# Kernel tuning notes

Measured on AMD Instinct MI355X. Metric: run time of the kernel, lower is better.

Reference implementation:

```python
import jax, jax.numpy as jnp
import numpy as np

N_IN = 100000
N_OUT = 5000
N_EDGES = 200000
FILTERS = 4
BATCH = 128


def setup_inputs() -> dict:
    key = jax.random.key(0)
    k1, k2, k3, k4 = jax.random.split(key, 4)
    x = jax.random.normal(k1, (BATCH, N_IN), dtype=jnp.float32)
    weight = jax.random.normal(k2, (N_EDGES, FILTERS), dtype=jnp.float32) * 0.01
    bias = jnp.zeros((N_OUT, FILTERS), dtype=jnp.float32)
    rows = jax.random.randint(k3, (N_EDGES,), 0, N_IN)
    cols = jax.random.randint(k4, (N_EDGES,), 0, N_OUT)
    return {"x": x, "weight": weight, "bias": bias, "rows": rows, "cols": cols}


def reference(x, weight, bias, rows, cols):
    # Sparse locally-connected layer: out[b,o,f] = sum_{e: cols[e]==o} x[b, rows[e]] * weight[e, f]
    # (equivalent to the original dense einsum 'bi,iof->bof' with the scattered weight tensor,
    #  but computed directly on the COO edge list)
    xg = x[:, rows]                                   # (B, E) gather per edge
    contrib = xg[:, :, None] * weight[None, :, :]     # (B, E, F)
    out = jnp.zeros((x.shape[0], N_OUT, FILTERS), dtype=x.dtype)
    out = out.at[:, cols, :].add(contrib)             # scatter-add to output nodes
    out = out + bias[None, :, :]
    return jax.nn.relu(out)
```

## Files before the change

kernel.cpp:

```cpp
#include <hip/hip_runtime.h>

#define N_IN 100000
#define N_OUT 5000
#define N_EDGES 200000
#define NB 128
#define CAP 128
#define T_TILES 3125
#define S_BLOCKS 782

__device__ __forceinline__ unsigned short f2bf_rne(float f) {
    unsigned int u = __float_as_uint(f);
    u += 0x7FFF + ((u >> 16) & 1);
    return (unsigned short)(u >> 16);
}

__global__ __launch_bounds__(256) void fused_prep(
    const float* __restrict__ x, unsigned short* __restrict__ xTb,
    const int* __restrict__ rows, const int* __restrict__ cols,
    int* __restrict__ count, int2* __restrict__ edge_pack) {
    __shared__ float tile[32][129];
    int t = threadIdx.x;
    if (blockIdx.x < T_TILES) {
        int n0 = blockIdx.x * 32;
        int q = t & 7;
        int brow = t >> 3;
#pragma unroll
        for (int p = 0; p < 4; ++p) {
            int b = brow + 32 * p;
            float4 v = *(const float4*)(x + (size_t)b * N_IN + n0 + 4 * q);
            tile[4 * q + 0][b] = v.x;
            tile[4 * q + 1][b] = v.y;
            tile[4 * q + 2][b] = v.z;
            tile[4 * q + 3][b] = v.w;
        }
        __syncthreads();
        int s = t & 31;
        int r = t >> 5;
#pragma unroll
        for (int p = 0; p < 4; ++p) {
            int nl = r + 8 * p;
            ushort4 o;
            o.x = f2bf_rne(tile[nl][4 * s + 0]);
            o.y = f2bf_rne(tile[nl][4 * s + 1]);
            o.z = f2bf_rne(tile[nl][4 * s + 2]);
            o.w = f2bf_rne(tile[nl][4 * s + 3]);
            *(ushort4*)(xTb + (size_t)(n0 + nl) * NB + 4 * s) = o;
        }
    } else {
        int e = (blockIdx.x - T_TILES) * 256 + t;
        if (e < N_EDGES) {
            int c = cols[e];
            int pos = atomicAdd(&count[c], 1);
            if (pos < CAP) edge_pack[c * CAP + pos] = make_int2(rows[e], e);
        }
    }
}

__device__ __forceinline__ void ld_step(unsigned int u, float4 wt, float4& a0, float4& a1) {
    float xa = __uint_as_float(u << 16);
    float xb = __uint_as_float(u & 0xFFFF0000u);
    a0.x = fmaf(xa, wt.x, a0.x); a0.y = fmaf(xa, wt.y, a0.y);
    a0.z = fmaf(xa, wt.z, a0.z); a0.w = fmaf(xa, wt.w, a0.w);
    a1.x = fmaf(xb, wt.x, a1.x); a1.y = fmaf(xb, wt.y, a1.y);
    a1.z = fmaf(xb, wt.z, a1.z); a1.w = fmaf(xb, wt.w, a1.w);
}

__global__ __launch_bounds__(256) void ld1d_main(
    const unsigned int* __restrict__ xg,
    const float4* __restrict__ bias4, const float4* __restrict__ w4,
    const int* __restrict__ count, const int2* __restrict__ edge_pack,
    float4* __restrict__ out4) {
    __shared__ int2 s_pack[4][CAP];
    int t = threadIdx.x;
    int wv = t >> 6;
    int l = t & 63;
    int c = blockIdx.x * 4 + wv;
    int cnt = count[c];
    cnt = (cnt < CAP) ? cnt : CAP;
    if (l < cnt) s_pack[wv][l] = edge_pack[c * CAP + l];
    if (l + 64 < cnt) s_pack[wv][l + 64] = edge_pack[c * CAP + l + 64];
    __syncthreads();
    float4 a0 = bias4[c];
    float4 a1 = a0;
    int k = 0;
    for (; k + 4 <= cnt; k += 4) {
        int2 p0 = s_pack[wv][k], p1 = s_pack[wv][k + 1];
        int2 p2 = s_pack[wv][k + 2], p3 = s_pack[wv][k + 3];
        unsigned int u0 = xg[(size_t)p0.x * 64 + l];
        unsigned int u1 = xg[(size_t)p1.x * 64 + l];
        unsigned int u2 = xg[(size_t)p2.x * 64 + l];
        unsigned int u3 = xg[(size_t)p3.x * 64 + l];
        float4 w0 = w4[p0.y], w1 = w4[p1.y], w2 = w4[p2.y], w3 = w4[p3.y];
        ld_step(u0, w0, a0, a1);
        ld_step(u1, w1, a0, a1);
        ld_step(u2, w2, a0, a1);
        ld_step(u3, w3, a0, a1);
    }
    for (; k < cnt; ++k) {
        int2 p = s_pack[wv][k];
        unsigned int u = xg[(size_t)p.x * 64 + l];
        float4 w = w4[p.y];
        ld_step(u, w, a0, a1);
    }
    a0.x = fmaxf(a0.x, 0.f); a0.y = fmaxf(a0.y, 0.f);
    a0.z = fmaxf(a0.z, 0.f); a0.w = fmaxf(a0.w, 0.f);
    a1.x = fmaxf(a1.x, 0.f); a1.y = fmaxf(a1.y, 0.f);
    a1.z = fmaxf(a1.z, 0.f); a1.w = fmaxf(a1.w, 0.f);
    out4[(size_t)(2 * l) * N_OUT + c] = a0;
    out4[(size_t)(2 * l + 1) * N_OUT + c] = a1;
}

extern "C" void kernel_launch(void* const* d_in, const int* in_sizes, int n_in,
                              void* d_out, int out_size, void* d_ws, size_t ws_size,
                              hipStream_t stream) {
    const float* x      = (const float*)d_in[0];
    const float* weight = (const float*)d_in[1];
    const float* bias   = (const float*)d_in[2];
    const int*   rows   = (const int*)d_in[3];
    const int*   cols   = (const int*)d_in[4];

    char* ws = (char*)d_ws;
    unsigned short* xTb  = (unsigned short*)(ws + 0);
    int2* edge_pack = (int2*)(ws + 25600000);
    int*  count     = (int*)(ws + 30720000);

    hipMemsetAsync(count, 0, N_OUT * sizeof(int), stream);

    fused_prep<<<T_TILES + S_BLOCKS, 256, 0, stream>>>(x, xTb, rows, cols, count, edge_pack);

    ld1d_main<<<N_OUT / 4, 256, 0, stream>>>((const unsigned int*)xTb, (const float4*)bias,
                                             (const float4*)weight, count, edge_pack,
                                             (float4*)d_out);
}
```

Before: 126.9 us.

## Split each output node across two wavefronts and reorder prep blocks

The main kernel now gives each output node two wavefronts that take alternate edges and combine partial sums through shared memory, with an 8-way unrolled gather loop. This doubles the block count and the memory-level parallelism per node, at the cost of an extra barrier and an LDS reduction. The prep kernel puts the edge-bucketing blocks first so the atomics start early, and it reads the transpose tile with float4 LDS loads using a padded stride of 132.

After: 131.4 us. 3.5% more time.

```diff
diff --git a/kernel.cpp b/kernel.cpp
--- a/kernel.cpp
+++ b/kernel.cpp
@@ -7,6 +7,7 @@
 #define CAP 128
 #define T_TILES 3125
 #define S_BLOCKS 782
+#define LDSW 132
 
 __device__ __forceinline__ unsigned short f2bf_rne(float f) {
     unsigned int u = __float_as_uint(f);
@@ -14,14 +15,30 @@
     return (unsigned short)(u >> 16);
 }
 
+__device__ __forceinline__ void ld_step(unsigned int u, float4 wt, float4& a0, float4& a1) {
+    float xa = __uint_as_float(u << 16);
+    float xb = __uint_as_float(u & 0xFFFF0000u);
+    a0.x = fmaf(xa, wt.x, a0.x); a0.y = fmaf(xa, wt.y, a0.y);
+    a0.z = fmaf(xa, wt.z, a0.z); a0.w = fmaf(xa, wt.w, a0.w);
+    a1.x = fmaf(xb, wt.x, a1.x); a1.y = fmaf(xb, wt.y, a1.y);
+    a1.z = fmaf(xb, wt.z, a1.z); a1.w = fmaf(xb, wt.w, a1.w);
+}
+
 __global__ __launch_bounds__(256) void fused_prep(
     const float* __restrict__ x, unsigned short* __restrict__ xTb,
     const int* __restrict__ rows, const int* __restrict__ cols,
     int* __restrict__ count, int2* __restrict__ edge_pack) {
-    __shared__ float tile[32][129];
+    __shared__ float tile[32][LDSW];
     int t = threadIdx.x;
-    if (blockIdx.x < T_TILES) {
-        int n0 = blockIdx.x * 32;
+    if (blockIdx.x < S_BLOCKS) {
+        int e = blockIdx.x * 256 + t;
+        if (e < N_EDGES) {
+            int c = cols[e];
+            int pos = atomicAdd(&count[c], 1);
+            if (pos < CAP) edge_pack[c * CAP + pos] = make_int2(rows[e], e);
+        }
+    } else {
+        int n0 = (blockIdx.x - S_BLOCKS) * 32;
         int q = t & 7;
         int brow = t >> 3;
 #pragma unroll
@@ -39,30 +56,15 @@
 #pragma unroll
         for (int p = 0; p < 4; ++p) {
             int nl = r + 8 * p;
+            float4 f = *(const float4*)&tile[nl][4 * s];
             ushort4 o;
-            o.x = f2bf_rne(tile[nl][4 * s + 0]);
-            o.y = f2bf_rne(tile[nl][4 * s + 1]);
-            o.z = f2bf_rne(tile[nl][4 * s + 2]);
-            o.w = f2bf_rne(tile[nl][4 * s + 3]);
+            o.x = f2bf_rne(f.x);
+            o.y = f2bf_rne(f.y);
+            o.z = f2bf_rne(f.z);
+            o.w = f2bf_rne(f.w);
             *(ushort4*)(xTb + (size_t)(n0 + nl) * NB + 4 * s) = o;
         }
-    } else {
-        int e = (blockIdx.x - T_TILES) * 256 + t;
-        if (e < N_EDGES) {
-            int c = cols[e];
-            int pos = atomicAdd(&count[c], 1);
-            if (pos < CAP) edge_pack[c * CAP + pos] = make_int2(rows[e], e);
-        }
     }
-}
-
-__device__ __forceinline__ void ld_step(unsigned int u, float4 wt, float4& a0, float4& a1) {
-    float xa = __uint_as_float(u << 16);
-    float xb = __uint_as_float(u & 0xFFFF0000u);
-    a0.x = fmaf(xa, wt.x, a0.x); a0.y = fmaf(xa, wt.y, a0.y);
-    a0.z = fmaf(xa, wt.z, a0.z); a0.w = fmaf(xa, wt.w, a0.w);
-    a1.x = fmaf(xb, wt.x, a1.x); a1.y = fmaf(xb, wt.y, a1.y);
-    a1.z = fmaf(xb, wt.z, a1.z); a1.w = fmaf(xb, wt.w, a1.w);
 }
 
 __global__ __launch_bounds__(256) void ld1d_main(
@@ -70,44 +72,68 @@
     const float4* __restrict__ bias4, const float4* __restrict__ w4,
     const int* __restrict__ count, const int2* __restrict__ edge_pack,
     float4* __restrict__ out4) {
-    __shared__ int2 s_pack[4][CAP];
+    __shared__ int2 s_pack[2][CAP];
+    __shared__ float4 s_part[2][64][2];
     int t = threadIdx.x;
-    int wv = t >> 6;
+    int w = t >> 6;
+    int cw = w >> 1;
+    int h = w & 1;
     int l = t & 63;
-    int c = blockIdx.x * 4 + wv;
+    int c = blockIdx.x * 2 + cw;
     int cnt = count[c];
     cnt = (cnt < CAP) ? cnt : CAP;
-    if (l < cnt) s_pack[wv][l] = edge_pack[c * CAP + l];
-    if (l + 64 < cnt) s_pack[wv][l + 64] = edge_pack[c * CAP + l + 64];
+    {
+        int idx = h * 64 + l;
+        if (idx < cnt) s_pack[cw][idx] = edge_pack[c * CAP + idx];
+    }
     __syncthreads();
-    float4 a0 = bias4[c];
-    float4 a1 = a0;
-    int k = 0;
-    for (; k + 4 <= cnt; k += 4) {
-        int2 p0 = s_pack[wv][k], p1 = s_pack[wv][k + 1];
-        int2 p2 = s_pack[wv][k + 2], p3 = s_pack[wv][k + 3];
+    float4 a0, a1;
+    if (h == 0) { a0 = bias4[c]; } else { a0 = make_float4(0.f, 0.f, 0.f, 0.f); }
+    a1 = a0;
+    int k = h;
+    for (; k + 14 < cnt; k += 16) {
+        int2 p0 = s_pack[cw][k],      p1 = s_pack[cw][k + 2];
+        int2 p2 = s_pack[cw][k + 4],  p3 = s_pack[cw][k + 6];
+        int2 p4 = s_pack[cw][k + 8],  p5 = s_pack[cw][k + 10];
+        int2 p6 = s_pack[cw][k + 12], p7 = s_pack[cw][k + 14];
         unsigned int u0 = xg[(size_t)p0.x * 64 + l];
         unsigned int u1 = xg[(size_t)p1.x * 64 + l];
         unsigned int u2 = xg[(size_t)p2.x * 64 + l];
         unsigned int u3 = xg[(size_t)p3.x * 64 + l];
+        unsigned int u4 = xg[(size_t)p4.x * 64 + l];
+        unsigned int u5 = xg[(size_t)p5.x * 64 + l];
+        unsigned int u6 = xg[(size_t)p6.x * 64 + l];
+        unsigned int u7 = xg[(size_t)p7.x * 64 + l];
         float4 w0 = w4[p0.y], w1 = w4[p1.y], w2 = w4[p2.y], w3 = w4[p3.y];
-        ld_step(u0, w0, a0, a1);
-        ld_step(u1, w1, a0, a1);
-        ld_step(u2, w2, a0, a1);
-        ld_step(u3, w3, a0, a1);
+        float4 wq = w4[p4.y], w5 = w4[p5.y], w6 = w4[p6.y], w7 = w4[p7.y];
+        ld_step(u0, w0, a0, a1); ld_step(u1, w1, a0, a1);
+        ld_step(u2, w2, a0, a1); ld_step(u3, w3, a0, a1);
+        ld_step(u4, wq, a0, a1); ld_step(u5, w5, a0, a1);
+        ld_step(u6, w6, a0, a1); ld_step(u7, w7, a0, a1);
     }
-    for (; k < cnt; ++k) {
-        int2 p = s_pack[wv][k];
+    for (; k < cnt; k += 2) {
+        int2 p = s_pack[cw][k];
         unsigned int u = xg[(size_t)p.x * 64 + l];
-        float4 w = w4[p.y];
-        ld_step(u, w, a0, a1);
+        float4 wt = w4[p.y];
+        ld_step(u, wt, a0, a1);
     }
-    a0.x = fmaxf(a0.x, 0.f); a0.y = fmaxf(a0.y, 0.f);
-    a0.z = fmaxf(a0.z, 0.f); a0.w = fmaxf(a0.w, 0.f);
-    a1.x = fmaxf(a1.x, 0.f); a1.y = fmaxf(a1.y, 0.f);
-    a1.z = fmaxf(a1.z, 0.f); a1.w = fmaxf(a1.w, 0.f);
-    out4[(size_t)(2 * l) * N_OUT + c] = a0;
-    out4[(size_t)(2 * l + 1) * N_OUT + c] = a1;
+    if (h == 1) {
+        s_part[cw][l][0] = a0;
+        s_part[cw][l][1] = a1;
+    }
+    __syncthreads();
+    if (h == 0) {
+        float4 q0 = s_part[cw][l][0];
+        float4 q1 = s_part[cw][l][1];
+        a0.x += q0.x; a0.y += q0.y; a0.z += q0.z; a0.w += q0.w;
+        a1.x += q1.x; a1.y += q1.y; a1.z += q1.z; a1.w += q1.w;
+        a0.x = fmaxf(a0.x, 0.f); a0.y = fmaxf(a0.y, 0.f);
+        a0.z = fmaxf(a0.z, 0.f); a0.w = fmaxf(a0.w, 0.f);
+        a1.x = fmaxf(a1.x, 0.f); a1.y = fmaxf(a1.y, 0.f);
+        a1.z = fmaxf(a1.z, 0.f); a1.w = fmaxf(a1.w, 0.f);
+        out4[(size_t)(2 * l) * N_OUT + c] = a0;
+        out4[(size_t)(2 * l + 1) * N_OUT + c] = a1;
+    }
 }
 
 extern "C" void kernel_launch(void* const* d_in, const int* in_sizes, int n_in,
@@ -120,15 +146,15 @@
     const int*   cols   = (const int*)d_in[4];
 
     char* ws = (char*)d_ws;
-    unsigned short* xTb  = (unsigned short*)(ws + 0);
+    unsigned short* xTb = (unsigned short*)(ws + 0);
     int2* edge_pack = (int2*)(ws + 25600000);
     int*  count     = (int*)(ws + 30720000);
 
     hipMemsetAsync(count, 0, N_OUT * sizeof(int), stream);
 
-    fused_prep<<<T_TILES + S_BLOCKS, 256, 0, stream>>>(x, xTb, rows, cols, count, edge_pack);
+    fused_prep<<<S_BLOCKS + T_TILES, 256, 0, stream>>>(x, xTb, rows, cols, count, edge_pack);
 
-    ld1d_main<<<N_OUT / 4, 256, 0, stream>>>((const unsigned int*)xTb, (const float4*)bias,
+    ld1d_main<<<N_OUT / 2, 256, 0, stream>>>((const unsigned int*)xTb, (const float4*)bias,
                                              (const float4*)weight, count, edge_pack,
                                              (float4*)d_out);
 }
```
